# Kernel tuning notes

Measured on AMD Instinct MI355X. Metric: run time of the kernel, lower is better.

## Reference

```python
import jax, jax.numpy as jnp
import numpy as np

B, S, D, H = 2, 2048, 1024, 16
HD = D // H  # 64

def setup_inputs() -> dict:
    key = jax.random.key(0)
    k1, k2, k3, k4, k5 = jax.random.split(key, 5)
    scale = 0.02
    return {
        "hidden_states": jax.random.normal(k1, (B, S, D), dtype=jnp.float32),
        "w_attn": jax.random.normal(k2, (D, 3 * D), dtype=jnp.float32) * scale,
        "b_attn": jax.random.normal(k3, (3 * D,), dtype=jnp.float32) * scale,
        "w_proj": jax.random.normal(k4, (D, D), dtype=jnp.float32) * scale,
        "b_proj": jax.random.normal(k5, (D,), dtype=jnp.float32) * scale,
    }

def reference(hidden_states, w_attn, b_attn, w_proj, b_proj):
    # qkv projection: [B,S,3D] -> split
    qkv = hidden_states @ w_attn + b_attn
    q, k, v = jnp.split(qkv, 3, axis=-1)
    # split heads -> [B,H,S,HD]
    def split_heads(t):
        return t.reshape(B, S, H, HD).transpose(0, 2, 1, 3)
    q, k, v = split_heads(q), split_heads(k), split_heads(v)
    # eager attention: full [B,H,S,S] scores, causal mask, softmax, AV
    scores = jnp.einsum('bhqd,bhkd->bhqk', q, k) / jnp.sqrt(jnp.float32(HD))
    causal = jnp.tril(jnp.ones((S, S), dtype=bool))  # [S,S]
    mask_value = jnp.finfo(scores.dtype).min
    scores = jnp.where(causal[None, None], scores, mask_value)
    attn = jax.nn.softmax(scores, axis=-1)
    out = jnp.einsum('bhqk,bhkd->bhqd', attn, v)
    # merge heads -> [B,S,D], output projection
    out = out.transpose(0, 2, 1, 3).reshape(B, S, D)
    out = out @ w_proj + b_proj
    return out
```

## Files before the change

### kernel.cpp

```cpp
#include <hip/hip_runtime.h>
#include <hip/hip_bf16.h>
#include <math.h>
#include <stdint.h>

typedef unsigned short u16;
typedef __attribute__((ext_vector_type(8))) short bf16x8;
typedef __attribute__((ext_vector_type(4))) float f32x4;

#define MFMA16(A,B,C) __builtin_amdgcn_mfma_f32_16x16x32_bf16(A,B,C,0,0,0)
#define EXP2F(x) __builtin_amdgcn_exp2f(x)

#define BB 2
#define SS 2048
#define NT (BB*SS)

__device__ __forceinline__ u16 f2bf(float f) {
    union { float f; unsigned u; } c; c.f = f;
    unsigned r = c.u + 0x7FFF + ((c.u >> 16) & 1);
    return (u16)(r >> 16);
}
__device__ __forceinline__ float bf2f(u16 v) {
    union { unsigned u; float f; } c; c.u = ((unsigned)v) << 16;
    return c.f;
}

__device__ __forceinline__ void gl_lds16(const u16* g, u16* l) {
    __builtin_amdgcn_global_load_lds(
        (const __attribute__((address_space(1))) void*)(uintptr_t)g,
        (__attribute__((address_space(3))) void*)(uintptr_t)l, 16, 0, 0);
}

__global__ __launch_bounds__(256) void prep(const float* __restrict__ hs,
                                            const float* __restrict__ wa,
                                            const float* __restrict__ wp,
                                            u16* __restrict__ hsb,
                                            u16* __restrict__ waT,
                                            u16* __restrict__ wpT) {
    __shared__ float tile[64][65];
    const int bid = blockIdx.x;
    const int t = threadIdx.x;
    if (bid < 4096) {
        int i = (bid * 256 + t) * 4;
        float4 v = *(const float4*)&hs[i];
        ushort4 o;
        o.x = f2bf(v.x); o.y = f2bf(v.y); o.z = f2bf(v.z); o.w = f2bf(v.w);
        *(ushort4*)&hsb[i] = o;
        return;
    }
    const int r = bid - 4096;
    const int k0 = (r & 15) * 64;
    const int by = r >> 4;
    const bool isA = by < 48;
    const int m0 = (isA ? by : by - 48) * 64;
    const int M = isA ? 3072 : 1024;
    const float* in = isA ? wa : wp;
    u16* out = isA ? waT : wpT;
    #pragma unroll
    for (int rep = 0; rep < 16; ++rep) {
        int idx = rep * 256 + t;
        int kk = idx >> 6, mm = idx & 63;
        tile[kk][mm] = in[(size_t)(k0 + kk) * M + m0 + mm];
    }
    __syncthreads();
    #pragma unroll
    for (int rep = 0; rep < 16; ++rep) {
        int idx = rep * 256 + t;
        int mm = idx >> 6, kk = idx & 63;
        out[(size_t)(m0 + mm) * 1024 + k0 + kk] = f2bf(tile[kk][mm]);
    }
}

template<int MD, typename OutT, bool FUSE_V>
__global__ __launch_bounds__(256) void gemm_bt(const u16* __restrict__ A,
                                               const u16* __restrict__ BT,
                                               const float* __restrict__ bias,
                                               OutT* __restrict__ C,
                                               u16* __restrict__ vtg) {
    __shared__ u16 As[2][128 * 32];
    __shared__ u16 Bs[2][128 * 32];
    const int n0 = blockIdx.x * 128;
    const int m0 = blockIdx.y * 128;
    const int t = threadIdx.x;
    const int lane = t & 63;
    const int w = t >> 6;
    const int wr = (w >> 1) * 64, wc = (w & 1) * 64;
    const int ln = lane & 15, hi = lane >> 4;

    f32x4 acc[4][4];
    const f32x4 fz = {0.f, 0.f, 0.f, 0.f};
    #pragma unroll
    for (int i = 0; i < 4; ++i)
        #pragma unroll
        for (int j = 0; j < 4; ++j) acc[i][j] = fz;

    const int srow_in = lane >> 2;
    const int schunk  = lane & 3;

    #pragma unroll
    for (int p = 0; p < 2; ++p) {
        int q   = w * 2 + p;
        int row = q * 16 + srow_in;
        int cg  = schunk ^ ((row >> 1) & 3);
        gl_lds16(&A [(size_t)(n0 + row) * 1024 + cg * 8], &As[0][q * 512]);
        gl_lds16(&BT[(size_t)(m0 + row) * 1024 + cg * 8], &Bs[0][q * 512]);
    }

    for (int i = 0; i < 32; ++i) {
        const int cur = i & 1;
        __syncthreads();

        if (i < 31) {
            const int nxt = cur ^ 1;
            const int k0 = (i + 1) * 32;
            #pragma unroll
            for (int p = 0; p < 2; ++p) {
                int q   = w * 2 + p;
                int row = q * 16 + srow_in;
                int cg  = schunk ^ ((row >> 1) & 3);
                gl_lds16(&A [(size_t)(n0 + row) * 1024 + k0 + cg * 8], &As[nxt][q * 512]);
                gl_lds16(&BT[(size_t)(m0 + row) * 1024 + k0 + cg * 8], &Bs[nxt][q * 512]);
            }
        }

        bf16x8 af[4], bf[4];
        #pragma unroll
        for (int mi = 0; mi < 4; ++mi) {
            int r = wr + mi * 16 + ln;
            af[mi] = *(const bf16x8*)&As[cur][r * 32 + ((hi ^ ((r >> 1) & 3)) << 3)];
        }
        #pragma unroll
        for (int ni = 0; ni < 4; ++ni) {
            int r = wc + ni * 16 + ln;
            bf[ni] = *(const bf16x8*)&Bs[cur][r * 32 + ((hi ^ ((r >> 1) & 3)) << 3)];
        }
        __builtin_amdgcn_s_setprio(1);
        #pragma unroll
        for (int mi = 0; mi < 4; ++mi)
            #pragma unroll
            for (int ni = 0; ni < 4; ++ni)
                acc[mi][ni] = MFMA16(af[mi], bf[ni], acc[mi][ni]);
        __builtin_amdgcn_s_setprio(0);
    }

    #pragma unroll
    for (int mi = 0; mi < 4; ++mi) {
        #pragma unroll
        for (int ni = 0; ni < 4; ++ni) {
            int col = m0 + wc + ni * 16 + ln;
            float bv = bias[col];
            int row0 = n0 + wr + mi * 16 + hi * 4;
            if (FUSE_V && col >= 2048) {
                int b  = row0 >> 11;
                int s  = row0 & 2047;
                int kt = s >> 6, kl = s & 63;
                int h  = (col - 2048) >> 6, d = (col - 2048) & 63;
                int g    = (kl >> 5) * 4 + ((kl >> 2) & 3);
                int half = (kl >> 4) & 1;
                ushort4 ov;
                ov.x = f2bf(acc[mi][ni][0] + bv);
                ov.y = f2bf(acc[mi][ni][1] + bv);
                ov.z = f2bf(acc[mi][ni][2] + bv);
                ov.w = f2bf(acc[mi][ni][3] + bv);
                *(ushort4*)&vtg[(size_t)((b * 16 + h) * 32 + kt) * 4096 +
                                (size_t)(g * 64 + d) * 8 + half * 4] = ov;
            } else {
                #pragma unroll
                for (int r = 0; r < 4; ++r) {
                    float v = acc[mi][ni][r] + bv;
                    if constexpr (sizeof(OutT) == 4) C[(size_t)(row0 + r) * MD + col] = v;
                    else                             C[(size_t)(row0 + r) * MD + col] = (OutT)f2bf(v);
                }
            }
        }
    }
}

__global__ __launch_bounds__(256) void attn_mfma(const u16* __restrict__ qkv,
                                                 const u16* __restrict__ vtg,
                                                 u16* __restrict__ ctx) {
    __shared__ u16 Ks[2][64 * 64];
    __shared__ u16 Vs[2][64 * 64];
    const int bh = blockIdx.x;
    const int qt = 31 - blockIdx.y;
    const int b = bh >> 4, h = bh & 15;
    const int t = threadIdx.x, w = t >> 6, lane = t & 63;
    const int ln = lane & 15, hi = lane >> 4;
    const int qrow = qt * 64 + w * 16 + ln;
    const size_t tok = (size_t)b * SS;

    bf16x8 qb[2];
    #pragma unroll
    for (int t2 = 0; t2 < 2; ++t2) {
        bf16x8 v = *(const bf16x8*)&qkv[(tok + qrow) * 3072 + h * 64 + t2 * 32 + hi * 8];
        #pragma unroll
        for (int i = 0; i < 8; ++i)
            v[i] = (short)f2bf(bf2f((u16)v[i]) * 0.180336881f);
        qb[t2] = v;
    }

    float m_run = -1e30f;
    float l_run = 0.f;
    f32x4 o[4];
    const f32x4 fz = {0.f, 0.f, 0.f, 0.f};
    #pragma unroll
    for (int i = 0; i < 4; ++i) o[i] = fz;

    const int kkey_l = w * 8 + (lane >> 3);
    const int ksch   = lane & 7;
    const u16* vsrc  = vtg + ((size_t)bh * 32) * 4096;

    {
        const size_t kvb = tok * 3072 + h * 64;
        #pragma unroll
        for (int p = 0; p < 2; ++p) {
            int kk = p * 32 + kkey_l;
            gl_lds16(&qkv[kvb + (size_t)kk * 3072 + 1024 + ((ksch ^ (kk & 7)) << 3)],
                     &Ks[0][(p * 32 + w * 8) * 64]);
            gl_lds16(&vsrc[(size_t)((w * 2 + p) * 64 + lane) * 8],
                     &Vs[0][(w * 2 + p) * 512]);
        }
    }

    for (int kt = 0; kt <= qt; ++kt) {
        const int cur = kt & 1;
        __syncthreads();

        if (kt < qt) {
            const int nxt = cur ^ 1;
            const size_t kvb = (tok + (kt + 1) * 64) * 3072 + h * 64;
            const u16* vs2 = vsrc + (size_t)(kt + 1) * 4096;
            #pragma unroll
            for (int p = 0; p < 2; ++p) {
                int kk = p * 32 + kkey_l;
                gl_lds16(&qkv[kvb + (size_t)kk * 3072 + 1024 + ((ksch ^ (kk & 7)) << 3)],
                         &Ks[nxt][(p * 32 + w * 8) * 64]);
                gl_lds16(&vs2[(size_t)((w * 2 + p) * 64 + lane) * 8],
                         &Vs[nxt][(w * 2 + p) * 512]);
            }
        }

        f32x4 sacc[4];
        __builtin_amdgcn_s_setprio(1);
        #pragma unroll
        for (int s = 0; s < 4; ++s) {
            int key = s * 16 + ln;
            f32x4 a = fz;
            #pragma unroll
            for (int t2 = 0; t2 < 2; ++t2) {
                bf16x8 kf = *(const bf16x8*)&Ks[cur][key * 64 + (((t2 * 4 + hi) ^ (key & 7)) << 3)];
                a = MFMA16(kf, qb[t2], a);
            }
            sacc[s] = a;
        }
        __builtin_amdgcn_s_setprio(0);

        float p_[16];
        if (kt == qt) {
            #pragma unroll
            for (int s = 0; s < 4; ++s)
                #pragma unroll
                for (int r = 0; r < 4; ++r) {
                    int keyg = kt * 64 + s * 16 + hi * 4 + r;
                    p_[s * 4 + r] = (keyg <= qrow) ? sacc[s][r] : -1e30f;
                }
        } else {
            #pragma unroll
            for (int s = 0; s < 4; ++s)
                #pragma unroll
                for (int r = 0; r < 4; ++r)
                    p_[s * 4 + r] = sacc[s][r];
        }
        float mp = fmaxf(fmaxf(p_[0], p_[1]), p_[2]);
        mp = fmaxf(fmaxf(mp, p_[3]),  p_[4]);
        mp = fmaxf(fmaxf(mp, p_[5]),  p_[6]);
        mp = fmaxf(fmaxf(mp, p_[7]),  p_[8]);
        mp = fmaxf(fmaxf(mp, p_[9]),  p_[10]);
        mp = fmaxf(fmaxf(mp, p_[11]), p_[12]);
        mp = fmaxf(fmaxf(mp, p_[13]), p_[14]);
        mp = fmaxf(mp, p_[15]);

        if (!__all(mp - m_run <= 8.f)) {
            float mloc = fmaxf(mp, __shfl_xor(mp, 16));
            mloc = fmaxf(mloc, __shfl_xor(mloc, 32));
            float m_new = fmaxf(m_run, mloc);
            float alpha = EXP2F(m_run - m_new);
            l_run *= alpha;
            #pragma unroll
            for (int dt = 0; dt < 4; ++dt) o[dt] *= alpha;
            m_run = m_new;
        }
        float lsum = 0.f;
        #pragma unroll
        for (int i = 0; i < 16; ++i) {
            float e = EXP2F(p_[i] - m_run);
            p_[i] = e;
            lsum += e;
        }
        l_run += lsum;

        bf16x8 pa[2];
        #pragma unroll
        for (int k2 = 0; k2 < 2; ++k2) {
            union { unsigned wd[4]; bf16x8 v; } pu;
            #pragma unroll
            for (int qi = 0; qi < 4; ++qi)
                asm("v_cvt_pk_bf16_f32 %0, %1, %2"
                    : "=v"(pu.wd[qi])
                    : "v"(p_[k2 * 8 + 2 * qi]), "v"(p_[k2 * 8 + 2 * qi + 1]));
            pa[k2] = pu.v;
        }

        __builtin_amdgcn_s_setprio(1);
        #pragma unroll
        for (int dt = 0; dt < 4; ++dt)
            #pragma unroll
            for (int k2 = 0; k2 < 2; ++k2) {
                bf16x8 va = *(const bf16x8*)&Vs[cur][(size_t)((k2 * 4 + hi) * 64 + dt * 16 + ln) * 8];
                o[dt] = MFMA16(va, pa[k2], o[dt]);
            }
        __builtin_amdgcn_s_setprio(0);
    }

    float lt = l_run + __shfl_xor(l_run, 16);
    lt += __shfl_xor(lt, 32);
    float inv = 1.f / lt;
    #pragma unroll
    for (int dt = 0; dt < 4; ++dt) {
        ushort4 ov;
        ov.x = f2bf(o[dt][0] * inv);
        ov.y = f2bf(o[dt][1] * inv);
        ov.z = f2bf(o[dt][2] * inv);
        ov.w = f2bf(o[dt][3] * inv);
        *(ushort4*)&ctx[(tok + qrow) * 1024 + h * 64 + dt * 16 + hi * 4] = ov;
    }
}

extern "C" void kernel_launch(void* const* d_in, const int* in_sizes, int n_in,
                              void* d_out, int out_size, void* d_ws, size_t ws_size,
                              hipStream_t stream) {
    const float* hs     = (const float*)d_in[0];
    const float* w_attn = (const float*)d_in[1];
    const float* b_attn = (const float*)d_in[2];
    const float* w_proj = (const float*)d_in[3];
    const float* b_proj = (const float*)d_in[4];
    float* out = (float*)d_out;

    char* ws = (char*)d_ws;
    u16* hsb  = (u16*)ws;
    u16* waT  = (u16*)(ws + ((size_t)8  << 20));
    u16* wpT  = (u16*)(ws + ((size_t)14 << 20));
    u16* qkvb = (u16*)(ws + ((size_t)16 << 20));
    u16* ctxb = (u16*)(ws + ((size_t)40 << 20));
    u16* vtg  = (u16*)(ws + ((size_t)48 << 20));

    prep<<<5120, 256, 0, stream>>>(hs, w_attn, w_proj, hsb, waT, wpT);

    gemm_bt<3072, u16, true><<<dim3(32, 24), 256, 0, stream>>>(hsb, waT, b_attn, qkvb, vtg);
    attn_mfma<<<dim3(BB * 16, SS / 64), 256, 0, stream>>>(qkvb, vtg, ctxb);
    gemm_bt<1024, float, false><<<dim3(32, 8), 256, 0, stream>>>(ctxb, wpT, b_proj, out, nullptr);
}
```

Baseline: 95.86 us.

## Split long causal query tiles across two blocks and merge partial softmax results

Result: slower. 103.8 us, median of 3 (+8.3%).

```diff
diff --git a/kernel.cpp b/kernel.cpp
--- a/kernel.cpp
+++ b/kernel.cpp
@@ -175,13 +175,27 @@
     }
 }
 
-__global__ __launch_bounds__(256) void attn_mfma(const u16* __restrict__ qkv,
-                                                 const u16* __restrict__ vtg,
-                                                 u16* __restrict__ ctx) {
+__global__ __launch_bounds__(256, 8) void attn_mfma(const u16* __restrict__ qkv,
+                                                    const u16* __restrict__ vtg,
+                                                    u16* __restrict__ ctx,
+                                                    float* __restrict__ po,
+                                                    float* __restrict__ pm,
+                                                    float* __restrict__ pl) {
     __shared__ u16 Ks[2][64 * 64];
     __shared__ u16 Vs[2][64 * 64];
     const int bh = blockIdx.x;
-    const int qt = 31 - blockIdx.y;
+    const int y  = blockIdx.y;
+    int qt, part, k_lo, k_hi;
+    bool full;
+    if (y < 32) {
+        qt = 31 - (y >> 1); part = y & 1; full = false;
+        int n = qt + 1, half = (n + 1) >> 1;
+        k_lo = part ? half : 0;
+        k_hi = part ? n : half;
+    } else {
+        qt = 47 - y; part = 0; full = true;
+        k_lo = 0; k_hi = qt + 1;
+    }
     const int b = bh >> 4, h = bh & 15;
     const int t = threadIdx.x, w = t >> 6, lane = t & 63;
     const int ln = lane & 15, hi = lane >> 4;
@@ -210,24 +224,24 @@
     const u16* vsrc  = vtg + ((size_t)bh * 32) * 4096;
 
     {
-        const size_t kvb = tok * 3072 + h * 64;
+        const size_t kvb = (tok + (size_t)k_lo * 64) * 3072 + h * 64;
         #pragma unroll
         for (int p = 0; p < 2; ++p) {
             int kk = p * 32 + kkey_l;
             gl_lds16(&qkv[kvb + (size_t)kk * 3072 + 1024 + ((ksch ^ (kk & 7)) << 3)],
                      &Ks[0][(p * 32 + w * 8) * 64]);
-            gl_lds16(&vsrc[(size_t)((w * 2 + p) * 64 + lane) * 8],
+            gl_lds16(&vsrc[(size_t)k_lo * 4096 + (size_t)((w * 2 + p) * 64 + lane) * 8],
                      &Vs[0][(w * 2 + p) * 512]);
         }
     }
 
-    for (int kt = 0; kt <= qt; ++kt) {
-        const int cur = kt & 1;
+    for (int kt = k_lo; kt < k_hi; ++kt) {
+        const int cur = (kt - k_lo) & 1;
         __syncthreads();
 
-        if (kt < qt) {
+        if (kt + 1 < k_hi) {
             const int nxt = cur ^ 1;
-            const size_t kvb = (tok + (kt + 1) * 64) * 3072 + h * 64;
+            const size_t kvb = (tok + (size_t)(kt + 1) * 64) * 3072 + h * 64;
             const u16* vs2 = vsrc + (size_t)(kt + 1) * 4096;
             #pragma unroll
             for (int p = 0; p < 2; ++p) {
@@ -323,15 +337,61 @@
 
     float lt = l_run + __shfl_xor(l_run, 16);
     lt += __shfl_xor(lt, 32);
-    float inv = 1.f / lt;
-    #pragma unroll
-    for (int dt = 0; dt < 4; ++dt) {
+    if (full) {
+        float inv = 1.f / lt;
+        #pragma unroll
+        for (int dt = 0; dt < 4; ++dt) {
+            ushort4 ov;
+            ov.x = f2bf(o[dt][0] * inv);
+            ov.y = f2bf(o[dt][1] * inv);
+            ov.z = f2bf(o[dt][2] * inv);
+            ov.w = f2bf(o[dt][3] * inv);
+            *(ushort4*)&ctx[(tok + qrow) * 1024 + h * 64 + dt * 16 + hi * 4] = ov;
+        }
+    } else {
+        const int pidx = (bh * 16 + (qt - 16)) * 2 + part;
+        float* pob = po + (size_t)pidx * 4096;
+        const int qrl = w * 16 + ln;
+        #pragma unroll
+        for (int dt = 0; dt < 4; ++dt)
+            *(f32x4*)&pob[qrl * 64 + dt * 16 + hi * 4] = o[dt];
+        if (hi == 0) {
+            pm[pidx * 64 + qrl] = m_run;
+            pl[pidx * 64 + qrl] = lt;
+        }
+    }
+}
+
+__global__ __launch_bounds__(256) void attn_merge(const float* __restrict__ po,
+                                                  const float* __restrict__ pm,
+                                                  const float* __restrict__ pl,
+                                                  u16* __restrict__ ctx) {
+    const int bh = blockIdx.x;
+    const int q16 = blockIdx.y;
+    const int b = bh >> 4, h = bh & 15;
+    const int t = threadIdx.x;
+    const int r = t >> 2;
+    const int dc = (t & 3) * 16;
+    const int base = (bh * 16 + q16) * 2;
+    const float* o0 = po + (size_t)(base + 0) * 4096 + r * 64 + dc;
+    const float* o1 = po + (size_t)(base + 1) * 4096 + r * 64 + dc;
+    const float m0 = pm[(base + 0) * 64 + r], l0 = pl[(base + 0) * 64 + r];
+    const float m1 = pm[(base + 1) * 64 + r], l1 = pl[(base + 1) * 64 + r];
+    const float m = fmaxf(m0, m1);
+    const float s0 = EXP2F(m0 - m), s1 = EXP2F(m1 - m);
+    const float inv = 1.f / (l0 * s0 + l1 * s1);
+    const float a0 = s0 * inv, a1 = s1 * inv;
+    u16* dst = &ctx[((size_t)(b * SS + (16 + q16) * 64 + r)) * 1024 + h * 64 + dc];
+    #pragma unroll
+    for (int c = 0; c < 4; ++c) {
+        float4 v0 = *(const float4*)&o0[c * 4];
+        float4 v1 = *(const float4*)&o1[c * 4];
         ushort4 ov;
-        ov.x = f2bf(o[dt][0] * inv);
-        ov.y = f2bf(o[dt][1] * inv);
-        ov.z = f2bf(o[dt][2] * inv);
-        ov.w = f2bf(o[dt][3] * inv);
-        *(ushort4*)&ctx[(tok + qrow) * 1024 + h * 64 + dt * 16 + hi * 4] = ov;
+        ov.x = f2bf(v0.x * a0 + v1.x * a1);
+        ov.y = f2bf(v0.y * a0 + v1.y * a1);
+        ov.z = f2bf(v0.z * a0 + v1.z * a1);
+        ov.w = f2bf(v0.w * a0 + v1.w * a1);
+        *(ushort4*)&dst[c * 4] = ov;
     }
 }
 
@@ -352,10 +412,14 @@
     u16* qkvb = (u16*)(ws + ((size_t)16 << 20));
     u16* ctxb = (u16*)(ws + ((size_t)40 << 20));
     u16* vtg  = (u16*)(ws + ((size_t)48 << 20));
+    float* po = (float*)(ws + ((size_t)56 << 20));
+    float* pm = (float*)(ws + ((size_t)72 << 20));
+    float* pl = (float*)(ws + ((size_t)72 << 20) + (1 << 18));
 
     prep<<<5120, 256, 0, stream>>>(hs, w_attn, w_proj, hsb, waT, wpT);
 
     gemm_bt<3072, u16, true><<<dim3(32, 24), 256, 0, stream>>>(hsb, waT, b_attn, qkvb, vtg);
-    attn_mfma<<<dim3(BB * 16, SS / 64), 256, 0, stream>>>(qkvb, vtg, ctxb);
+    attn_mfma<<<dim3(BB * 16, 48), 256, 0, stream>>>(qkvb, vtg, ctxb, po, pm, pl);
+    attn_merge<<<dim3(BB * 16, 16), 256, 0, stream>>>(po, pm, pl, ctxb);
     gemm_bt<1024, float, false><<<dim3(32, 8), 256, 0, stream>>>(ctxb, wpT, b_proj, out, nullptr);
 }
```
